# Kernel tuning notes

Hardware: AMD Instinct MI355X
Metric: run time of the kernel (lower is better)

The kernel has to match this reference:

```python
import jax, jax.numpy as jnp
import numpy as np

EPS = 1e-6
NEG_INF = jnp.finfo(jnp.float32).min


def setup_inputs() -> dict:
    key = jax.random.key(0)
    ks = jax.random.split(key, 12)
    N, D, H, dh, F, V, L, B = 4, 1024, 16, 64, 4096, 32000, 2048, 1
    s = 0.02
    return {
        "x_BL": jax.random.randint(ks[0], (B, L), 0, V, dtype=jnp.int32),
        "embed": jax.random.normal(ks[1], (V, D), jnp.float32) * s,
        "pos_embed": jax.random.normal(ks[2], (L, D), jnp.float32) * s,
        "wq": jax.random.normal(ks[3], (N, D, H, dh), jnp.float32) * s,
        "wk": jax.random.normal(ks[4], (N, D, H, dh), jnp.float32) * s,
        "wv": jax.random.normal(ks[5], (N, D, H, dh), jnp.float32) * s,
        "wo": jax.random.normal(ks[6], (N, H, dh, D), jnp.float32) * s,
        "gate_w": jax.random.normal(ks[7], (N, D, F), jnp.float32) * s,
        "val_w": jax.random.normal(ks[8], (N, D, F), jnp.float32) * s,
        "ffn_out_w": jax.random.normal(ks[9], (N, F, D), jnp.float32) * s,
        "ln1_s": jnp.ones((N, D), jnp.float32),
        "ln2_s": jnp.ones((N, D), jnp.float32),
        "final_ln_s": jnp.ones((D,), jnp.float32),
    }


def rmsnorm(x, scale):
    var = jnp.mean(jnp.square(x), axis=-1, keepdims=True)
    return x * jax.lax.rsqrt(var + EPS) * scale


def attention(x_BLD, wq, wk, wv, wo):
    # wq/wk/wv: [D,H,dh]; wo: [H,dh,D]
    q = jnp.einsum('bld,dhk->blhk', x_BLD, wq)
    k = jnp.einsum('bld,dhk->blhk', x_BLD, wk)
    v = jnp.einsum('bld,dhk->blhk', x_BLD, wv)
    dh = wq.shape[-1]
    a = jnp.einsum('bqhd,bkhd->bhqk', q, k) / (dh ** 0.5)
    L = x_BLD.shape[1]
    mask = jnp.tril(jnp.ones((1, 1, L, L), dtype=jnp.bool_))
    a = jnp.where(mask, a, NEG_INF)
    a = jax.nn.softmax(a, axis=-1)
    o = jnp.einsum('bhqk,bkhd->bqhd', a, v)
    return jnp.einsum('bqhd,hdD->bqD', o, wo)


def ffn(x_BLD, gate_w, val_w, out_w):
    g = jax.nn.swish(jnp.einsum('bld,df->blf', x_BLD, gate_w))
    y = jnp.einsum('bld,df->blf', x_BLD, val_w) * g
    return jnp.einsum('blf,fd->bld', y, out_w)


def reference(x_BL, embed, pos_embed, wq, wk, wv, wo, gate_w, val_w,
              ffn_out_w, ln1_s, ln2_s, final_ln_s):
    x = embed[x_BL]                              # [B,L,D]
    L = x_BL.shape[1]
    x = x + pos_embed[jnp.arange(L)][None, :, :]
    N = wq.shape[0]
    for i in range(N):
        a = attention(rmsnorm(x, ln1_s[i]), wq[i], wk[i], wv[i], wo[i])
        f = ffn(rmsnorm(x, ln2_s[i]), gate_w[i], val_w[i], ffn_out_w[i])
        x = x + a + f
    x = rmsnorm(x, final_ln_s)
    logits = jnp.einsum('bld,vd->blv', x, embed)  # tied embedding attend
    return logits
```

## Files before the change

### kernel.cpp

```cpp
#include <hip/hip_runtime.h>
#include <cstdint>
#include <cstddef>

#define L_SEQ 2048
#define DMODEL 1024
#define NHEAD 16
#define DHEAD 64
#define FFN_F 4096
#define VOCAB 32000
#define NLAYER 4

typedef __attribute__((ext_vector_type(8))) short short8;
typedef __attribute__((ext_vector_type(4))) float f32x4;

__device__ __forceinline__ unsigned short f2bf(float f) {
  unsigned int u = __float_as_uint(f);
  u += 0x7fffu + ((u >> 16) & 1u);
  return (unsigned short)(u >> 16);
}
__device__ __forceinline__ float b2f(unsigned short h) {
  return __uint_as_float(((unsigned int)h) << 16);
}

__device__ __forceinline__ void glds16(const unsigned short* g, unsigned short* l) {
  __builtin_amdgcn_global_load_lds(
      (const __attribute__((address_space(1))) unsigned int*)g,
      (__attribute__((address_space(3))) unsigned int*)l, 16, 0, 0);
}

__device__ __forceinline__ float rmax16(float v) {
  v = fmaxf(v, __shfl_xor(v, 1));
  v = fmaxf(v, __shfl_xor(v, 2));
  v = fmaxf(v, __shfl_xor(v, 4));
  v = fmaxf(v, __shfl_xor(v, 8));
  return v;
}
__device__ __forceinline__ float rsum16(float v) {
  v += __shfl_xor(v, 1);
  v += __shfl_xor(v, 2);
  v += __shfl_xor(v, 4);
  v += __shfl_xor(v, 8);
  return v;
}

#define MFMA(ACC, AF, BF) \
  ACC = __builtin_amdgcn_mfma_f32_16x16x32_bf16(AF, BF, ACC, 0, 0, 0)

enum { E_F32 = 0, E_BF16 = 1, E_SWIGLU = 2, E_PART = 3 };

template <int EPI>
__global__ __launch_bounds__(512, 2) void gemm8p(
    const unsigned short* __restrict__ A, const unsigned short* __restrict__ B,
    void* __restrict__ Cg, int M, int N, int K, int lda, int ldb, int ldc,
    float alpha, int nby)
{
  const int nwg = gridDim.x;
  const int orig = blockIdx.x;
  const int q = nwg >> 3, r = nwg & 7;
  const int xcd = orig & 7, rest = orig >> 3;
  const int wgid = (xcd < r ? xcd * (q + 1) : r * (q + 1) + (xcd - r) * q) + rest;
  const int by = wgid % nby, bx = wgid / nby;
  const int mb = by * 256, nb = bx * 256;

  __shared__ __align__(16) unsigned short As_[2][256 * 64];
  __shared__ __align__(16) unsigned short Bs_[2][256 * 64];

  const int tid = threadIdx.x;
  const int lane = tid & 63;
  const int w = tid >> 6;
  const int wm = (w >> 2) * 128;
  const int wn = (w & 3) * 64;
  const int lr = lane & 15;
  const int lg = lane >> 4;
  const int srow = lane >> 3;
  const int scol = ((lane & 7) ^ srow) * 8;
  const int slot0 = (lg ^ (lr & 7)) * 8;
  const int slot1 = ((4 + lg) ^ (lr & 7)) * 8;

  f32x4 acc[8][4];
#pragma unroll
  for (int i = 0; i < 8; i++)
#pragma unroll
    for (int j = 0; j < 4; j++) acc[i][j] = (f32x4){0.f, 0.f, 0.f, 0.f};

  const unsigned short* Ab = A + (size_t)(mb + srow) * lda + scol;
  const unsigned short* Bb = B + (size_t)(nb + srow) * ldb + scol;

  auto stageA = [&](int t, int R) {
    const int s = t & 1, kb = t << 6;
#pragma unroll
    for (int c = 0; c < 2; c++) {
      int cid = w * 2 + c;
      int rb = ((cid >> 3) << 7) + R * 64 + ((cid & 7) << 3);
      glds16(Ab + (size_t)rb * lda + kb, &As_[s][rb * 64]);
    }
  };
  auto stageB = [&](int t, int R) {
    const int s = t & 1, kb = t << 6;
#pragma unroll
    for (int c = 0; c < 2; c++) {
      int cid = w * 2 + c;
      int rb = ((cid >> 2) << 6) + R * 32 + ((cid & 3) << 3);
      glds16(Bb + (size_t)rb * ldb + kb, &Bs_[s][rb * 64]);
    }
  };

  const int nk = K >> 6;
  stageA(0, 0); stageA(0, 1); stageB(0, 0); stageB(0, 1);
  stageA(1, 0); stageB(1, 0); stageB(1, 1);
  asm volatile("s_waitcnt vmcnt(6)" ::: "memory");
  __builtin_amdgcn_s_barrier();

  short8 a[4][2], b0[2][2], b1[2][2];
#pragma unroll
  for (int j = 0; j < 2; j++) {
    b0[j][0] = *(const short8*)&Bs_[0][(wn + j * 16 + lr) * 64 + slot0];
    b0[j][1] = *(const short8*)&Bs_[0][(wn + j * 16 + lr) * 64 + slot1];
  }

  for (int t = 0; t < nk; ++t) {
    const int s = t & 1;
    const unsigned short* Asb = &As_[s][0];
    const unsigned short* Bsb = &Bs_[s][0];

#pragma unroll
    for (int i = 0; i < 4; i++) {
      a[i][0] = *(const short8*)&Asb[(wm + i * 16 + lr) * 64 + slot0];
      a[i][1] = *(const short8*)&Asb[(wm + i * 16 + lr) * 64 + slot1];
    }
    if (t + 1 < nk) stageA(t + 1, 1);
    __builtin_amdgcn_s_barrier();
    __builtin_amdgcn_s_setprio(1);
#pragma unroll
    for (int kk = 0; kk < 2; kk++)
#pragma unroll
      for (int i = 0; i < 4; i++)
#pragma unroll
        for (int j = 0; j < 2; j++) MFMA(acc[i][j], a[i][kk], b0[j][kk]);
    __builtin_amdgcn_s_setprio(0);
    __builtin_amdgcn_s_barrier();

#pragma unroll
    for (int j = 0; j < 2; j++) {
      b1[j][0] = *(const short8*)&Bsb[(wn + 32 + j * 16 + lr) * 64 + slot0];
      b1[j][1] = *(const short8*)&Bsb[(wn + 32 + j * 16 + lr) * 64 + slot1];
    }
    if (t + 2 < nk) stageA(t + 2, 0);
    __builtin_amdgcn_s_barrier();
    __builtin_amdgcn_s_setprio(1);
#pragma unroll
    for (int kk = 0; kk < 2; kk++)
#pragma unroll
      for (int i = 0; i < 4; i++)
#pragma unroll
        for (int j = 0; j < 2; j++) MFMA(acc[i][2 + j], a[i][kk], b1[j][kk]);
    __builtin_amdgcn_s_setprio(0);
    __builtin_amdgcn_s_barrier();

#pragma unroll
    for (int i = 0; i < 4; i++) {
      a[i][0] = *(const short8*)&Asb[(wm + 64 + i * 16 + lr) * 64 + slot0];
      a[i][1] = *(const short8*)&Asb[(wm + 64 + i * 16 + lr) * 64 + slot1];
    }
    if (t + 2 < nk) stageB(t + 2, 0);
    __builtin_amdgcn_s_barrier();
    __builtin_amdgcn_s_setprio(1);
#pragma unroll
    for (int kk = 0; kk < 2; kk++)
#pragma unroll
      for (int i = 0; i < 4; i++)
#pragma unroll
        for (int j = 0; j < 2; j++) MFMA(acc[4 + i][2 + j], a[i][kk], b1[j][kk]);
    __builtin_amdgcn_s_setprio(0);
    __builtin_amdgcn_s_barrier();

    if (t + 2 < nk) stageB(t + 2, 1);
    __builtin_amdgcn_s_barrier();
    __builtin_amdgcn_s_setprio(1);
#pragma unroll
    for (int kk = 0; kk < 2; kk++)
#pragma unroll
      for (int i = 0; i < 4; i++)
#pragma unroll
        for (int j = 0; j < 2; j++) MFMA(acc[4 + i][j], a[i][kk], b0[j][kk]);
    __builtin_amdgcn_s_setprio(0);
    if (t + 2 < nk) {
      asm volatile("s_waitcnt vmcnt(6)" ::: "memory");
    } else {
      asm volatile("s_waitcnt vmcnt(0)" ::: "memory");
    }
    __builtin_amdgcn_s_barrier();
    if (t + 1 < nk) {
      const unsigned short* Bn = &Bs_[s ^ 1][0];
#pragma unroll
      for (int j = 0; j < 2; j++) {
        b0[j][0] = *(const short8*)&Bn[(wn + j * 16 + lr) * 64 + slot0];
        b0[j][1] = *(const short8*)&Bn[(wn + j * 16 + lr) * 64 + slot1];
      }
    }
  }

#pragma unroll
  for (int i = 0; i < 8; i++) {
#pragma unroll
    for (int j = 0; j < 4; j++) {
      int oc = nb + wn + 16 * j + lr;
#pragma unroll
      for (int r4 = 0; r4 < 4; r4++) {
        int orow = mb + wm + 16 * i + lg * 4 + r4;
        float v = acc[i][j][r4] * alpha;
        if (EPI == E_F32) {
          ((float*)Cg)[(size_t)orow * ldc + oc] = v;
        } else if (EPI == E_BF16) {
          ((unsigned short*)Cg)[(size_t)orow * ldc + oc] = f2bf(v);
        } else if (EPI == E_SWIGLU) {
          float other = __shfl_xor(v, 1);
          float g = (lane & 1) ? other : v;
          float vv = (lane & 1) ? v : other;
          float sw = g / (1.0f + expf(-g)) * vv;
          if (!(lane & 1))
            ((unsigned short*)Cg)[(size_t)orow * ldc + (oc >> 1)] = f2bf(sw);
        }
      }
    }
  }
}

template <int EPI>
__global__ __launch_bounds__(256) void gemm_fast(
    const unsigned short* __restrict__ A, const unsigned short* __restrict__ B,
    void* __restrict__ Cg, int M, int N, int K, int lda, int ldb, int ldc,
    float alpha, int nbx)
{
  const int nwg = gridDim.x;
  const int orig = blockIdx.x;
  const int q = nwg >> 3, r = nwg & 7;
  const int xcd = orig & 7, rest = orig >> 3;
  const int wgid = (xcd < r ? xcd * (q + 1) : r * (q + 1) + (xcd - r) * q) + rest;
  const int bx = wgid % nbx, by = wgid / nbx;
  const int mb = by * 128;
  const int nb = bx * 128;

  const int Keff = (EPI == E_PART) ? (K >> 1) : K;
  const int koff = (EPI == E_PART) ? blockIdx.z * Keff : 0;

  __shared__ __align__(16) unsigned short As[2][128 * 64];
  __shared__ __align__(16) unsigned short Bs[2][128 * 64];

  const int tid = threadIdx.x;
  const int lane = tid & 63;
  const int wave = tid >> 6;
  const int wm = (wave >> 1) * 64;
  const int wn = (wave & 1) * 64;
  const int lr = lane & 15;
  const int lg = lane >> 4;

  const int srow = lane >> 3;
  const int scol = ((lane & 7) ^ srow) * 8;

  f32x4 acc[4][4];
#pragma unroll
  for (int i = 0; i < 4; i++)
#pragma unroll
    for (int j = 0; j < 4; j++) acc[i][j] = (f32x4){0.f, 0.f, 0.f, 0.f};

  const unsigned short* Abase = A + (size_t)(mb + wave * 32 + srow) * lda + koff + scol;
  const unsigned short* Bbase = B + (size_t)(nb + wave * 32 + srow) * ldb + koff + scol;

  auto stage = [&](int kb, int b) {
#pragma unroll
    for (int c = 0; c < 4; c++)
      glds16(Abase + (size_t)(c * 8) * lda + kb, &As[b][(wave * 32 + c * 8) * 64]);
#pragma unroll
    for (int c = 0; c < 4; c++)
      glds16(Bbase + (size_t)(c * 8) * ldb + kb, &Bs[b][(wave * 32 + c * 8) * 64]);
  };

  stage(0, 0);
  __syncthreads();
  int cur = 0;
  const int nk = Keff >> 6;

  for (int t = 0; t < nk; ++t) {
    if (t + 1 < nk) stage((t + 1) << 6, cur ^ 1);

    short8 af[2][4], bfb[2][4];
#pragma unroll
    for (int h = 0; h < 2; h++) {
      const int swz = ((h * 4 + lg) ^ (lr & 7)) * 8;
#pragma unroll
      for (int i = 0; i < 4; i++) {
        af[h][i] = *(const short8*)&As[cur][(wm + 16 * i + lr) * 64 + swz];
        bfb[h][i] = *(const short8*)&Bs[cur][(wn + 16 * i + lr) * 64 + swz];
      }
    }
#pragma unroll
    for (int h = 0; h < 2; h++)
#pragma unroll
      for (int i = 0; i < 4; i++)
#pragma unroll
        for (int j = 0; j < 4; j++) MFMA(acc[i][j], af[h][i], bfb[h][j]);

    __syncthreads();
    cur ^= 1;
  }

#pragma unroll
  for (int i = 0; i < 4; i++) {
#pragma unroll
    for (int j = 0; j < 4; j++) {
      int oc = nb + wn + 16 * j + lr;
#pragma unroll
      for (int r4 = 0; r4 < 4; r4++) {
        int orow = mb + wm + 16 * i + lg * 4 + r4;
        float v = acc[i][j][r4] * alpha;
        if (EPI == E_F32) {
          ((float*)Cg)[(size_t)orow * ldc + oc] = v;
        } else if (EPI == E_BF16) {
          ((unsigned short*)Cg)[(size_t)orow * ldc + oc] = f2bf(v);
        } else {
          float* C = (float*)Cg + (size_t)blockIdx.z * ((size_t)L_SEQ * DMODEL);
          C[(size_t)orow * ldc + oc] = v;
        }
      }
    }
  }
}

__global__ __launch_bounds__(128) void flash_attn(
    const unsigned short* __restrict__ Qg, const unsigned short* __restrict__ Kg,
    const unsigned short* __restrict__ Vt, unsigned short* __restrict__ Og,
    int ldq, int ldo)
{
  const int bid = blockIdx.x;
  const int slot = bid & 255, ph = bid >> 8;
  const int h = slot >> 4;
  const int qs = slot & 15;
  const int qb = ph ? (31 - qs) : qs;

  const int tid = threadIdx.x;
  const int lane = tid & 63;
  const int w = tid >> 6;
  const int lr = lane & 15;
  const int lg = lane >> 4;

  __shared__ __align__(16) unsigned short KsL[2][64 * 64];
  __shared__ __align__(16) unsigned short VsL[2][64 * 64];
  __shared__ __align__(16) unsigned short Ps[2][32 * 64];

  const int srow = lane >> 3;
  const int scol = ((lane & 7) ^ srow) * 8;

  short8 qf[2][2];
#pragma unroll
  for (int i = 0; i < 2; i++)
#pragma unroll
    for (int kk = 0; kk < 2; kk++)
      qf[i][kk] = *(const short8*)(Qg +
          (size_t)(qb * 64 + w * 32 + i * 16 + lr) * ldq + h * 64 + kk * 32 + lg * 8);

  f32x4 acc_o[2][4];
  float m_st[2][4], l_st[2][4];
#pragma unroll
  for (int i = 0; i < 2; i++)
#pragma unroll
    for (int j = 0; j < 4; j++) acc_o[i][j] = (f32x4){0.f, 0.f, 0.f, 0.f};
#pragma unroll
  for (int i = 0; i < 2; i++)
#pragma unroll
    for (int r = 0; r < 4; r++) { m_st[i][r] = -1e30f; l_st[i][r] = 0.f; }

  const int ntiles = qb + 1;
  const int qmin = qb * 64 + w * 32;

  auto stage = [&](int t, int buf) {
#pragma unroll
    for (int c = 0; c < 4; c++) {
      int row = w * 32 + c * 8 + srow;
      glds16(Kg + (size_t)(t * 64 + row) * ldq + h * 64 + scol,
             &KsL[buf][row * 64]);
      glds16(Vt + (size_t)(h * 64 + row) * L_SEQ + t * 64 + scol,
             &VsL[buf][row * 64]);
    }
  };

  stage(0, 0);
  __syncthreads();
  int buf = 0;

  for (int t = 0; t < ntiles; t++) {
    if (t + 1 < ntiles) stage(t + 1, buf ^ 1);

    f32x4 sa[2][4];
#pragma unroll
    for (int i = 0; i < 2; i++)
#pragma unroll
      for (int j = 0; j < 4; j++) sa[i][j] = (f32x4){0.f, 0.f, 0.f, 0.f};
#pragma unroll
    for (int kk = 0; kk < 2; kk++) {
      short8 kf[4];
#pragma unroll
      for (int j = 0; j < 4; j++)
        kf[j] = *(const short8*)&KsL[buf][(j * 16 + lr) * 64 + ((kk * 4 + lg) ^ (lr & 7)) * 8];
#pragma unroll
      for (int i = 0; i < 2; i++)
#pragma unroll
        for (int j = 0; j < 4; j++) MFMA(sa[i][j], qf[i][kk], kf[j]);
    }

    const bool diag = (t * 64 + 63) > qmin;
#pragma unroll
    for (int i = 0; i < 2; i++)
#pragma unroll
      for (int j = 0; j < 4; j++)
#pragma unroll
        for (int r = 0; r < 4; r++) {
          float s = sa[i][j][r] * 0.125f;
          if (diag) {
            int kg = t * 64 + j * 16 + lr;
            int qg = qmin + i * 16 + lg * 4 + r;
            if (kg > qg) s = -1e30f;
          }
          sa[i][j][r] = s;
        }

    float fsc[2][4], mnew[2][4];
#pragma unroll
    for (int i = 0; i < 2; i++)
#pragma unroll
      for (int r = 0; r < 4; r++) {
        float mx = fmaxf(fmaxf(sa[i][0][r], sa[i][1][r]), fmaxf(sa[i][2][r], sa[i][3][r]));
        mx = rmax16(mx);
        float mn = fmaxf(m_st[i][r], mx);
        mnew[i][r] = mn;
        fsc[i][r] = __expf(m_st[i][r] - mn);
        m_st[i][r] = mn;
      }
#pragma unroll
    for (int i = 0; i < 2; i++)
#pragma unroll
      for (int r = 0; r < 4; r++) {
        float ls = 0.f;
#pragma unroll
        for (int j = 0; j < 4; j++) {
          float p = __expf(sa[i][j][r] - mnew[i][r]);
          sa[i][j][r] = p;
          ls += p;
        }
        ls = rsum16(ls);
        l_st[i][r] = l_st[i][r] * fsc[i][r] + ls;
      }
#pragma unroll
    for (int i = 0; i < 2; i++)
#pragma unroll
      for (int j = 0; j < 4; j++)
#pragma unroll
        for (int r = 0; r < 4; r++) acc_o[i][j][r] *= fsc[i][r];

#pragma unroll
    for (int i = 0; i < 2; i++)
#pragma unroll
      for (int j = 0; j < 4; j++)
#pragma unroll
        for (int r = 0; r < 4; r++) {
          int qrl = lg * 4 + r;
          int idx = (i * 16 + qrl) * 64 + (((j * 2 + (lr >> 3)) ^ (qrl & 7)) * 8) + (lr & 7);
          Ps[w][idx] = f2bf(sa[i][j][r]);
        }

#pragma unroll
    for (int kk = 0; kk < 2; kk++) {
      short8 pf[2], vf[4];
#pragma unroll
      for (int i = 0; i < 2; i++)
        pf[i] = *(const short8*)&Ps[w][(i * 16 + lr) * 64 + ((kk * 4 + lg) ^ (lr & 7)) * 8];
#pragma unroll
      for (int j = 0; j < 4; j++)
        vf[j] = *(const short8*)&VsL[buf][(j * 16 + lr) * 64 + ((kk * 4 + lg) ^ (lr & 7)) * 8];
#pragma unroll
      for (int i = 0; i < 2; i++)
#pragma unroll
        for (int j = 0; j < 4; j++) MFMA(acc_o[i][j], pf[i], vf[j]);
    }

    __syncthreads();
    buf ^= 1;
  }

  float inv[2][4];
#pragma unroll
  for (int i = 0; i < 2; i++)
#pragma unroll
    for (int r = 0; r < 4; r++) inv[i][r] = 1.0f / l_st[i][r];
#pragma unroll
  for (int i = 0; i < 2; i++)
#pragma unroll
    for (int j = 0; j < 4; j++)
#pragma unroll
      for (int r = 0; r < 4; r++) {
        size_t row = qmin + i * 16 + lg * 4 + r;
        Og[row * ldo + h * 64 + j * 16 + lr] = f2bf(acc_o[i][j][r] * inv[i][r]);
      }
}

__global__ __launch_bounds__(256) void rmsnorm_fold(
    const float* __restrict__ xin,
    const float* __restrict__ p1, const float* __restrict__ p2,
    const float* __restrict__ s1, const float* __restrict__ s2,
    unsigned short* __restrict__ o1, unsigned short* __restrict__ o2,
    float* __restrict__ xout, int fold)
{
  int row = blockIdx.x;
  int tid = threadIdx.x;
  float v[4];
  float ss = 0.f;
#pragma unroll
  for (int i = 0; i < 4; i++) {
    size_t idx = (size_t)row * DMODEL + tid + 256 * i;
    float val = xin[idx];
    if (fold) {
      val += p1[idx] + p2[idx];
      xout[idx] = val;
    }
    v[i] = val;
    ss += val * val;
  }
#pragma unroll
  for (int o = 32; o > 0; o >>= 1) ss += __shfl_xor(ss, o);
  __shared__ float red[4];
  if ((tid & 63) == 0) red[tid >> 6] = ss;
  __syncthreads();
  ss = red[0] + red[1] + red[2] + red[3];
  float inv = rsqrtf(ss / DMODEL + 1e-6f);
#pragma unroll
  for (int i = 0; i < 4; i++) {
    int d = tid + 256 * i;
    size_t idx = (size_t)row * DMODEL + d;
    float nv = v[i] * inv;
    o1[idx] = f2bf(nv * s1[d]);
    if (o2) o2[idx] = f2bf(nv * s2[d]);
  }
}

__global__ __launch_bounds__(256) void prep_weights(
    const float* __restrict__ wq, const float* __restrict__ wk,
    const float* __restrict__ wv, const float* __restrict__ wo,
    const float* __restrict__ gw, const float* __restrict__ vw,
    const float* __restrict__ fw,
    unsigned short* __restrict__ qkvw, unsigned short* __restrict__ wft,
    unsigned short* __restrict__ gvt)
{
  __shared__ float t0[32][33], t1[32][33];
  int bid = blockIdx.x;
  int tx = threadIdx.x, ty = threadIdx.y;
  if (bid < 4096) {
    int j = bid >> 10, tile = bid & 1023;
    int c0 = (tile & 31) * 32, r0 = (tile >> 5) * 32;
    const float* src = j == 0 ? wq : j == 1 ? wk : j == 2 ? wv : wo;
#pragma unroll
    for (int k = 0; k < 32; k += 8)
      t0[ty + k][tx] = src[(size_t)(r0 + ty + k) * 1024 + c0 + tx];
    __syncthreads();
    unsigned short* dst;
    int ldd;
    if (j < 3) { dst = qkvw + (size_t)j * 1024 * 1024; ldd = 1024; }
    else { dst = wft; ldd = 5120; }
#pragma unroll
    for (int k = 0; k < 32; k += 8)
      dst[(size_t)(c0 + ty + k) * ldd + r0 + tx] = f2bf(t0[tx][ty + k]);
  } else if (bid < 8192) {
    int tile = bid - 4096;
    int c0 = (tile & 31) * 32;
    int r0 = (tile >> 5) * 32;
#pragma unroll
    for (int k = 0; k < 32; k += 8)
      t0[ty + k][tx] = fw[(size_t)(r0 + ty + k) * 1024 + c0 + tx];
    __syncthreads();
#pragma unroll
    for (int k = 0; k < 32; k += 8)
      wft[(size_t)(c0 + ty + k) * 5120 + 1024 + r0 + tx] = f2bf(t0[tx][ty + k]);
  } else {
    int tile = bid - 8192;
    int c0 = (tile & 127) * 32;
    int d0 = (tile >> 7) * 32;
#pragma unroll
    for (int k = 0; k < 32; k += 8) {
      t0[ty + k][tx] = gw[(size_t)(d0 + ty + k) * 4096 + c0 + tx];
      t1[ty + k][tx] = vw[(size_t)(d0 + ty + k) * 4096 + c0 + tx];
    }
    __syncthreads();
#pragma unroll
    for (int k = 0; k < 32; k += 8) {
      gvt[(size_t)(2 * (c0 + ty + k)) * 1024 + d0 + tx] = f2bf(t0[tx][ty + k]);
      gvt[(size_t)(2 * (c0 + ty + k) + 1) * 1024 + d0 + tx] = f2bf(t1[tx][ty + k]);
    }
  }
}

__global__ __launch_bounds__(256) void transpose_act(
    const unsigned short* __restrict__ in, unsigned short* __restrict__ out,
    int ld_in, int ld_out)
{
  __shared__ float tile[32][33];
  int c0 = blockIdx.x * 32;
  int r0 = blockIdx.y * 32;
  int tx = threadIdx.x;
  int ty = threadIdx.y;
#pragma unroll
  for (int j = 0; j < 32; j += 8)
    tile[ty + j][tx] = b2f(in[(size_t)(r0 + ty + j) * ld_in + c0 + tx]);
  __syncthreads();
#pragma unroll
  for (int j = 0; j < 32; j += 8)
    out[(size_t)(c0 + ty + j) * ld_out + r0 + tx] = f2bf(tile[tx][ty + j]);
}

__global__ __launch_bounds__(256) void convert_f2b_kernel(
    const float* __restrict__ in, unsigned short* __restrict__ out, size_t n)
{
  size_t i = ((size_t)blockIdx.x * 256 + threadIdx.x) * 4;
  if (i + 3 < n) {
    float4 v = *(const float4*)(in + i);
    out[i] = f2bf(v.x);
    out[i + 1] = f2bf(v.y);
    out[i + 2] = f2bf(v.z);
    out[i + 3] = f2bf(v.w);
  }
}

__global__ __launch_bounds__(256) void embed_kernel(
    const int* __restrict__ ids, const float* __restrict__ emb,
    const float* __restrict__ pos, float* __restrict__ x)
{
  int l = blockIdx.x;
  int id = ids[l];
#pragma unroll
  for (int i = 0; i < 4; i++) {
    int d = threadIdx.x + 256 * i;
    x[(size_t)l * DMODEL + d] = emb[(size_t)id * DMODEL + d] + pos[(size_t)l * DMODEL + d];
  }
}

extern "C" void kernel_launch(void* const* d_in, const int* in_sizes, int n_in,
                              void* d_out, int out_size, void* d_ws, size_t ws_size,
                              hipStream_t stream)
{
  const int L = L_SEQ, D = DMODEL, F = FFN_F, V = VOCAB;
  const int* ids = (const int*)d_in[0];
  const float* embed = (const float*)d_in[1];
  const float* pos = (const float*)d_in[2];
  const float* wq = (const float*)d_in[3];
  const float* wk = (const float*)d_in[4];
  const float* wv = (const float*)d_in[5];
  const float* wo = (const float*)d_in[6];
  const float* gatew = (const float*)d_in[7];
  const float* valw = (const float*)d_in[8];
  const float* ffow = (const float*)d_in[9];
  const float* ln1 = (const float*)d_in[10];
  const float* ln2 = (const float*)d_in[11];
  const float* lnf = (const float*)d_in[12];

  char* ws = (char*)d_ws;
  size_t off = 0;
  auto alloc = [&](size_t bytes) -> void* {
    void* p = ws + off;
    off += (bytes + 255) & ~(size_t)255;
    return p;
  };
  float* x = (float*)alloc((size_t)L * D * 4);
  float* pbuf = (float*)alloc((size_t)2 * L * D * 4);
  unsigned short* xn1 = (unsigned short*)alloc((size_t)L * D * 2);
  unsigned short* xn2 = (unsigned short*)alloc((size_t)L * D * 2);
  unsigned short* qkvb = (unsigned short*)alloc((size_t)L * 3 * D * 2);
  unsigned short* vtb = (unsigned short*)alloc((size_t)L * D * 2);
  unsigned short* ohb = (unsigned short*)alloc((size_t)L * 5120 * 2);
  unsigned short* qkvw = (unsigned short*)alloc((size_t)3 * D * D * 2);
  unsigned short* wft = (unsigned short*)alloc((size_t)D * 5120 * 2);
  unsigned short* gvt = (unsigned short*)alloc((size_t)2 * F * D * 2);
  unsigned short* embb = (unsigned short*)alloc((size_t)V * D * 2);

  dim3 blk(256);
  dim3 blk512(512);
  dim3 blkT(32, 8);

  embed_kernel<<<L, blk, 0, stream>>>(ids, embed, pos, x);
  convert_f2b_kernel<<<(unsigned)((size_t)V * D / 1024), blk, 0, stream>>>(embed, embb, (size_t)V * D);

  for (int i = 0; i < NLAYER; i++) {
    prep_weights<<<12288, blkT, 0, stream>>>(
        wq + (size_t)i * D * D, wk + (size_t)i * D * D, wv + (size_t)i * D * D,
        wo + (size_t)i * D * D, gatew + (size_t)i * D * F, valw + (size_t)i * D * F,
        ffow + (size_t)i * F * D, qkvw, wft, gvt);

    rmsnorm_fold<<<L, blk, 0, stream>>>(x, pbuf, pbuf + (size_t)L * D,
                                        ln1 + (size_t)i * D, ln2 + (size_t)i * D,
                                        xn1, xn2, x, i > 0 ? 1 : 0);

    gemm_fast<E_BF16><<<dim3(24 * 16), blk, 0, stream>>>(
        xn1, qkvw, qkvb, L, 3 * D, D, D, D, 3 * D, 1.0f, 24);

    transpose_act<<<dim3(D / 32, L / 32), blkT, 0, stream>>>(qkvb + 2 * D, vtb, 3 * D, L);

    flash_attn<<<dim3(512), dim3(128), 0, stream>>>(qkvb, qkvb + D, vtb, ohb, 3 * D, 5120);

    gemm8p<E_SWIGLU><<<dim3(8 * 32), blk512, 0, stream>>>(
        xn2, gvt, ohb + 1024, L, 2 * F, D, D, D, 5120, 1.0f, 8);

    gemm_fast<E_PART><<<dim3(8 * 16, 1, 2), blk, 0, stream>>>(
        ohb, wft, pbuf, L, D, 5120, 5120, 5120, D, 1.0f, 8);
  }

  rmsnorm_fold<<<L, blk, 0, stream>>>(x, pbuf, pbuf + (size_t)L * D,
                                      lnf, nullptr, xn1, nullptr, x, 1);
  gemm8p<E_F32><<<dim3(8 * 125), blk512, 0, stream>>>(
      xn1, embb, d_out, L, V, D, D, D, V, 1.0f, 8);
}
```

Before: 1.188 ms.

## Fold RMSNorm scales into weights and fuse QKV with SwiGLU GEMM

The per-column RMSNorm scales (ln1, ln2, final) are folded into the bf16 weight conversion, so rmsnorm writes one unscaled normalized activation instead of two scaled copies. The QKV projection and the gate/value SwiGLU projection then share the same input and run as one wide gemm8p launch (N=11264), made possible by placing qkvw and gvt next to each other in the workspace. The epilogue splits output columns between the QKV buffer and the SwiGLU output. This removes a kernel launch and one activation buffer and fills the GPU better with a single larger grid, at the cost of a branchy epilogue and a dependency on buffer adjacency.

Result: slower. 1.327 ms (+11.7%).

```diff
diff --git a/kernel.cpp b/kernel.cpp
--- a/kernel.cpp
+++ b/kernel.cpp
@@ -46,12 +46,13 @@
 #define MFMA(ACC, AF, BF) \
   ACC = __builtin_amdgcn_mfma_f32_16x16x32_bf16(AF, BF, ACC, 0, 0, 0)
 
-enum { E_F32 = 0, E_BF16 = 1, E_SWIGLU = 2, E_PART = 3 };
+enum { E_F32 = 0, E_BF16 = 1, E_QKVSWI = 2, E_PART = 3 };
 
 template <int EPI>
 __global__ __launch_bounds__(512, 2) void gemm8p(
     const unsigned short* __restrict__ A, const unsigned short* __restrict__ B,
-    void* __restrict__ Cg, int M, int N, int K, int lda, int ldb, int ldc,
+    void* __restrict__ Cg, void* __restrict__ Cg2,
+    int M, int N, int K, int lda, int ldb, int ldc,
     float alpha, int nby)
 {
   const int nwg = gridDim.x;
@@ -213,13 +214,17 @@
           ((float*)Cg)[(size_t)orow * ldc + oc] = v;
         } else if (EPI == E_BF16) {
           ((unsigned short*)Cg)[(size_t)orow * ldc + oc] = f2bf(v);
-        } else if (EPI == E_SWIGLU) {
-          float other = __shfl_xor(v, 1);
-          float g = (lane & 1) ? other : v;
-          float vv = (lane & 1) ? v : other;
-          float sw = g / (1.0f + expf(-g)) * vv;
-          if (!(lane & 1))
-            ((unsigned short*)Cg)[(size_t)orow * ldc + (oc >> 1)] = f2bf(sw);
+        } else if (EPI == E_QKVSWI) {
+          if (oc < 3072) {
+            ((unsigned short*)Cg)[(size_t)orow * 3072 + oc] = f2bf(v);
+          } else {
+            float other = __shfl_xor(v, 1);
+            float g = (lane & 1) ? other : v;
+            float vv = (lane & 1) ? v : other;
+            float sw = g / (1.0f + expf(-g)) * vv;
+            if (!(lane & 1))
+              ((unsigned short*)Cg2)[(size_t)orow * 5120 + ((oc - 3072) >> 1)] = f2bf(sw);
+          }
         }
       }
     }
@@ -506,9 +511,7 @@
 __global__ __launch_bounds__(256) void rmsnorm_fold(
     const float* __restrict__ xin,
     const float* __restrict__ p1, const float* __restrict__ p2,
-    const float* __restrict__ s1, const float* __restrict__ s2,
-    unsigned short* __restrict__ o1, unsigned short* __restrict__ o2,
-    float* __restrict__ xout, int fold)
+    unsigned short* __restrict__ o1, float* __restrict__ xout, int fold)
 {
   int row = blockIdx.x;
   int tid = threadIdx.x;
@@ -534,11 +537,8 @@
   float inv = rsqrtf(ss / DMODEL + 1e-6f);
 #pragma unroll
   for (int i = 0; i < 4; i++) {
-    int d = tid + 256 * i;
-    size_t idx = (size_t)row * DMODEL + d;
-    float nv = v[i] * inv;
-    o1[idx] = f2bf(nv * s1[d]);
-    if (o2) o2[idx] = f2bf(nv * s2[d]);
+    size_t idx = (size_t)row * DMODEL + tid + 256 * i;
+    o1[idx] = f2bf(v[i] * inv);
   }
 }
 
@@ -546,7 +546,8 @@
     const float* __restrict__ wq, const float* __restrict__ wk,
     const float* __restrict__ wv, const float* __restrict__ wo,
     const float* __restrict__ gw, const float* __restrict__ vw,
-    const float* __restrict__ fw,
+    const float* __restrict__ fw, const float* __restrict__ s1,
+    const float* __restrict__ s2,
     unsigned short* __restrict__ qkvw, unsigned short* __restrict__ wft,
     unsigned short* __restrict__ gvt)
 {
@@ -561,13 +562,17 @@
     for (int k = 0; k < 32; k += 8)
       t0[ty + k][tx] = src[(size_t)(r0 + ty + k) * 1024 + c0 + tx];
     __syncthreads();
-    unsigned short* dst;
-    int ldd;
-    if (j < 3) { dst = qkvw + (size_t)j * 1024 * 1024; ldd = 1024; }
-    else { dst = wft; ldd = 5120; }
-#pragma unroll
-    for (int k = 0; k < 32; k += 8)
-      dst[(size_t)(c0 + ty + k) * ldd + r0 + tx] = f2bf(t0[tx][ty + k]);
+    if (j < 3) {
+      unsigned short* dst = qkvw + (size_t)j * 1024 * 1024;
+      float sc = s1[r0 + tx];
+#pragma unroll
+      for (int k = 0; k < 32; k += 8)
+        dst[(size_t)(c0 + ty + k) * 1024 + r0 + tx] = f2bf(t0[tx][ty + k] * sc);
+    } else {
+#pragma unroll
+      for (int k = 0; k < 32; k += 8)
+        wft[(size_t)(c0 + ty + k) * 5120 + r0 + tx] = f2bf(t0[tx][ty + k]);
+    }
   } else if (bid < 8192) {
     int tile = bid - 4096;
     int c0 = (tile & 31) * 32;
@@ -589,10 +594,11 @@
       t1[ty + k][tx] = vw[(size_t)(d0 + ty + k) * 4096 + c0 + tx];
     }
     __syncthreads();
+    float sc = s2[d0 + tx];
 #pragma unroll
     for (int k = 0; k < 32; k += 8) {
-      gvt[(size_t)(2 * (c0 + ty + k)) * 1024 + d0 + tx] = f2bf(t0[tx][ty + k]);
-      gvt[(size_t)(2 * (c0 + ty + k) + 1) * 1024 + d0 + tx] = f2bf(t1[tx][ty + k]);
+      gvt[(size_t)(2 * (c0 + ty + k)) * 1024 + d0 + tx] = f2bf(t0[tx][ty + k] * sc);
+      gvt[(size_t)(2 * (c0 + ty + k) + 1) * 1024 + d0 + tx] = f2bf(t1[tx][ty + k] * sc);
     }
   }
 }
@@ -615,16 +621,18 @@
     out[(size_t)(c0 + ty + j) * ld_out + r0 + tx] = f2bf(tile[tx][ty + j]);
 }
 
-__global__ __launch_bounds__(256) void convert_f2b_kernel(
-    const float* __restrict__ in, unsigned short* __restrict__ out, size_t n)
+__global__ __launch_bounds__(256) void convert_embb(
+    const float* __restrict__ in, const float* __restrict__ lnf,
+    unsigned short* __restrict__ out, size_t n)
 {
   size_t i = ((size_t)blockIdx.x * 256 + threadIdx.x) * 4;
   if (i + 3 < n) {
     float4 v = *(const float4*)(in + i);
-    out[i] = f2bf(v.x);
-    out[i + 1] = f2bf(v.y);
-    out[i + 2] = f2bf(v.z);
-    out[i + 3] = f2bf(v.w);
+    int d = (int)(i & 1023);
+    out[i] = f2bf(v.x * lnf[d]);
+    out[i + 1] = f2bf(v.y * lnf[d + 1]);
+    out[i + 2] = f2bf(v.z * lnf[d + 2]);
+    out[i + 3] = f2bf(v.w * lnf[d + 3]);
   }
 }
 
@@ -669,14 +677,13 @@
   };
   float* x = (float*)alloc((size_t)L * D * 4);
   float* pbuf = (float*)alloc((size_t)2 * L * D * 4);
-  unsigned short* xn1 = (unsigned short*)alloc((size_t)L * D * 2);
-  unsigned short* xn2 = (unsigned short*)alloc((size_t)L * D * 2);
+  unsigned short* xhat = (unsigned short*)alloc((size_t)L * D * 2);
   unsigned short* qkvb = (unsigned short*)alloc((size_t)L * 3 * D * 2);
   unsigned short* vtb = (unsigned short*)alloc((size_t)L * D * 2);
   unsigned short* ohb = (unsigned short*)alloc((size_t)L * 5120 * 2);
   unsigned short* qkvw = (unsigned short*)alloc((size_t)3 * D * D * 2);
+  unsigned short* gvt = (unsigned short*)alloc((size_t)2 * F * D * 2);
   unsigned short* wft = (unsigned short*)alloc((size_t)D * 5120 * 2);
-  unsigned short* gvt = (unsigned short*)alloc((size_t)2 * F * D * 2);
   unsigned short* embb = (unsigned short*)alloc((size_t)V * D * 2);
 
   dim3 blk(256);
@@ -684,34 +691,32 @@
   dim3 blkT(32, 8);
 
   embed_kernel<<<L, blk, 0, stream>>>(ids, embed, pos, x);
-  convert_f2b_kernel<<<(unsigned)((size_t)V * D / 1024), blk, 0, stream>>>(embed, embb, (size_t)V * D);
+  convert_embb<<<(unsigned)((size_t)V * D / 1024), blk, 0, stream>>>(
+      embed, lnf, embb, (size_t)V * D);
 
   for (int i = 0; i < NLAYER; i++) {
     prep_weights<<<12288, blkT, 0, stream>>>(
         wq + (size_t)i * D * D, wk + (size_t)i * D * D, wv + (size_t)i * D * D,
         wo + (size_t)i * D * D, gatew + (size_t)i * D * F, valw + (size_t)i * D * F,
-        ffow + (size_t)i * F * D, qkvw, wft, gvt);
+        ffow + (size_t)i * F * D, ln1 + (size_t)i * D, ln2 + (size_t)i * D,
+        qkvw, wft, gvt);
 
     rmsnorm_fold<<<L, blk, 0, stream>>>(x, pbuf, pbuf + (size_t)L * D,
-                                        ln1 + (size_t)i * D, ln2 + (size_t)i * D,
-                                        xn1, xn2, x, i > 0 ? 1 : 0);
-
-    gemm_fast<E_BF16><<<dim3(24 * 16), blk, 0, stream>>>(
-        xn1, qkvw, qkvb, L, 3 * D, D, D, D, 3 * D, 1.0f, 24);
+                                        xhat, x, i > 0 ? 1 : 0);
+
+    gemm8p<E_QKVSWI><<<dim3(8 * 44), blk512, 0, stream>>>(
+        xhat, qkvw, qkvb, ohb + 1024, L, 11264, D, D, D, 3 * D, 1.0f, 8);
 
     transpose_act<<<dim3(D / 32, L / 32), blkT, 0, stream>>>(qkvb + 2 * D, vtb, 3 * D, L);
 
     flash_attn<<<dim3(512), dim3(128), 0, stream>>>(qkvb, qkvb + D, vtb, ohb, 3 * D, 5120);
-
-    gemm8p<E_SWIGLU><<<dim3(8 * 32), blk512, 0, stream>>>(
-        xn2, gvt, ohb + 1024, L, 2 * F, D, D, D, 5120, 1.0f, 8);
 
     gemm_fast<E_PART><<<dim3(8 * 16, 1, 2), blk, 0, stream>>>(
         ohb, wft, pbuf, L, D, 5120, 5120, 5120, D, 1.0f, 8);
   }
 
   rmsnorm_fold<<<L, blk, 0, stream>>>(x, pbuf, pbuf + (size_t)L * D,
-                                      lnf, nullptr, xn1, nullptr, x, 1);
+                                      xhat, x, 1);
   gemm8p<E_F32><<<dim3(8 * 125), blk512, 0, stream>>>(
-      xn1, embb, d_out, L, V, D, D, D, V, 1.0f, 8);
-}
+      xhat, embb, d_out, nullptr, L, V, D, D, D, V, 1.0f, 8);
+}
```
